# Optimization experiments

Measured on AMD Instinct MI355X. Metric: run time of the kernel, lower is better.

Reference implementation:

```python
import jax, jax.numpy as jnp
import numpy as np

# atom_dict indices
N_IDX, CA_IDX, C_IDX = 0, 1, 2
O4P_IDX, C2P_IDX, C1P_IDX = 11, 14, 15
NA_REF_IDX = 15  # C1'
TOP_K = 30
NUM_RBF = 16
MAX_REL = 32
NUM_POLY = 3
B, L, A = 1, 512, 24


def setup_inputs() -> dict:
    key = jax.random.key(0)
    ks = jax.random.split(key, 8)
    X = 5.0 * jax.random.normal(ks[0], (B, L, A, 3), dtype=jnp.float32)
    mask = jnp.ones((B, L), dtype=jnp.float32)
    R_idx = jnp.broadcast_to(jnp.arange(L, dtype=jnp.int32), (B, L))
    chain_labels = jnp.broadcast_to((jnp.arange(L) // (L // 2)).astype(jnp.int32), (B, L))
    X_m = jnp.ones((B, L, A), dtype=jnp.float32)
    R_polymer_type = jax.random.randint(ks[1], (B, L), 0, NUM_POLY)
    protein_mask = (R_polymer_type == 0).astype(jnp.float32)
    dna_mask = (R_polymer_type == 1).astype(jnp.float32)
    rna_mask = (R_polymer_type == 2).astype(jnp.float32)
    TOTAL_ATOMS = A + 2
    edge_in = 2 * MAX_REL + 2  # placeholder; real edge_in below
    edge_in = NUM_RBF * TOTAL_ATOMS * TOTAL_ATOMS + 16  # 10832
    W_pos = 0.1 * jax.random.normal(ks[2], (16, 2 * MAX_REL + 2), dtype=jnp.float32)
    b_pos = 0.01 * jax.random.normal(ks[3], (16,), dtype=jnp.float32)
    W_edge = 0.02 * jax.random.normal(ks[4], (128, edge_in), dtype=jnp.float32)
    W_node = 0.1 * jax.random.normal(ks[5], (128, NUM_POLY), dtype=jnp.float32)
    gamma_e = jnp.ones((128,), jnp.float32); beta_e = jnp.zeros((128,), jnp.float32)
    gamma_n = jnp.ones((128,), jnp.float32); beta_n = jnp.zeros((128,), jnp.float32)
    return dict(X=X, mask=mask, R_idx=R_idx, chain_labels=chain_labels, X_m=X_m,
                protein_mask=protein_mask, dna_mask=dna_mask, rna_mask=rna_mask,
                R_polymer_type=R_polymer_type, W_pos=W_pos, b_pos=b_pos,
                W_edge=W_edge, W_node=W_node, gamma_e=gamma_e, beta_e=beta_e,
                gamma_n=gamma_n, beta_n=beta_n)


def _get_cb(n, ca, c, wa, wb, wc):
    b = ca - n
    cc = c - ca
    a = jnp.cross(b, cc)
    return wa * a + wb * b + wc * cc + ca


def _layernorm(x, g, b, eps=1e-5):
    m = x.mean(-1, keepdims=True)
    v = ((x - m) ** 2).mean(-1, keepdims=True)
    return (x - m) / jnp.sqrt(v + eps) * g + b


def _dist_topk(Xc, mask):
    # Xc: [B,L,3]
    mask2d = mask[:, None, :] * mask[:, :, None]  # [B,L,L]
    dX = Xc[:, None, :, :] - Xc[:, :, None, :]
    D = mask2d * jnp.sqrt((dX ** 2).sum(-1) + 1e-6)
    D_max = D.max(-1, keepdims=True)
    D_adjust = D + (1.0 - mask2d) * D_max
    negD, E_idx = jax.lax.top_k(-D_adjust, TOP_K)  # smallest distances
    return -negD, E_idx


def reference(X, mask, R_idx, chain_labels, X_m, protein_mask, dna_mask, rna_mask,
              R_polymer_type, W_pos, b_pos, W_edge, W_node, gamma_e, beta_e,
              gamma_n, beta_n):
    Bb, Ll = X.shape[0], X.shape[1]
    Ca = X[:, :, CA_IDX]
    Nb = X[:, :, N_IDX]
    Cc = X[:, :, C_IDX]
    Cb = _get_cb(Nb, Ca, Cc, -0.58273431, 0.56802827, -0.54067466)
    na_ref = X[:, :, NA_REF_IDX]
    N_na = _get_cb(X[:, :, O4P_IDX], X[:, :, C1P_IDX], X[:, :, C2P_IDX],
                   -0.56967352, 0.51055973, -0.53122153)
    aug_X = jnp.concatenate([X, Cb[:, :, None, :], N_na[:, :, None, :]], axis=2)  # [B,L,26,3]
    aug_Xm = jnp.concatenate([X_m, protein_mask[:, :, None],
                              (rna_mask + dna_mask)[:, :, None]], axis=-1)  # [B,L,26]

    _, E_idx = _dist_topk(Ca + na_ref, mask)  # [B,L,K]

    # gather neighbor atoms / masks: [B,L,K,26,3], [B,L,K,26]
    bidx = jnp.arange(Bb)[:, None, None]
    X_g = aug_X[bidx, E_idx]
    Xm_g = aug_Xm[bidx, E_idx]

    # all-atom pairwise distances [B,L,K,26,26]
    Dall = jnp.sqrt(((aug_X[:, :, None, :, None, :] - X_g[:, :, :, None, :, :]) ** 2).sum(-1) + 1e-6)
    D_mu = jnp.linspace(2.0, 22.0, NUM_RBF)
    D_sigma = (22.0 - 2.0) / NUM_RBF
    RBF = jnp.exp(-((Dall[..., None] - D_mu) / D_sigma) ** 2)  # [B,L,K,26,26,16]
    RBF = RBF * aug_Xm[:, :, None, :, None, None] * Xm_g[:, :, :, None, :, None]
    RBF_all = RBF.reshape(Bb, Ll, TOP_K, -1)  # [B,L,K,26*26*16]

    offset = R_idx[:, :, None] - R_idx[:, None, :]  # [B,L,L]
    offset = jnp.take_along_axis(offset, E_idx, axis=2)  # [B,L,K]
    d_chains = (chain_labels[:, :, None] == chain_labels[:, None, :]).astype(jnp.int32)
    E_chains = jnp.take_along_axis(d_chains, E_idx, axis=2)

    d = jnp.clip(offset + MAX_REL, 0, 2 * MAX_REL) * E_chains + (1 - E_chains) * (2 * MAX_REL + 1)
    d_onehot = jax.nn.one_hot(d, 2 * MAX_REL + 2, dtype=jnp.float32)
    E_positional = d_onehot @ W_pos.T + b_pos  # [B,L,K,16]

    E = jnp.concatenate([E_positional, RBF_all], axis=-1)
    E = E @ W_edge.T  # [B,L,K,128]
    E = _layernorm(E, gamma_e, beta_e)

    V = jax.nn.one_hot(R_polymer_type, NUM_POLY, dtype=jnp.float32) @ W_node.T
    V = _layernorm(V, gamma_n, beta_n)
    return V, E, E_idx
```

## Files before the change

### kernel.cpp

```cpp
#include <hip/hip_runtime.h>
#include <stdint.h>


#define NRES   512
#define TOPK   30
#define NATOM  26
#define KTOT   10832
#define NDCP   170
#define MTOT   (NRES*TOPK)
#define NOUT   128
#define KSPLIT 6

#define OFF_AUGX4  0u
#define OFF_EIDX   212992u
#define OFF_WSWZ   274432u
#define OFF_JTAB   1667072u
#define OFF_EPART  4861952u

#define OUT_V     0
#define OUT_E     (NRES*NOUT)
#define OUT_EIDX  (OUT_E + MTOT*NOUT)

typedef __attribute__((ext_vector_type(4))) float f32x4;

#define SA_C   0.96089792702915984f
#define MU0_C  1.9217958540583197f
#define MUS_C  1.2811972360388798f

__device__ __forceinline__ unsigned short f2bf(float f) {
    unsigned u = __builtin_bit_cast(unsigned, f);
    return (unsigned short)((u + 0x7fffu + ((u >> 16) & 1u)) >> 16);
}
__device__ __forceinline__ float bf2f(unsigned short u) {
    return __builtin_bit_cast(float, (unsigned)u << 16);
}
__device__ __forceinline__ float bflo(unsigned u) {
    return __builtin_bit_cast(float, u << 16);
}
__device__ __forceinline__ float bfhi(unsigned u) {
    return __builtin_bit_cast(float, u & 0xffff0000u);
}
__device__ __forceinline__ unsigned long long shfl_xor_u64(unsigned long long v, int m) {
    unsigned lo = (unsigned)v, hi = (unsigned)(v >> 32);
    lo = (unsigned)__shfl_xor((int)lo, m, 64);
    hi = (unsigned)__shfl_xor((int)hi, m, 64);
    return ((unsigned long long)hi << 32) | lo;
}
__device__ __forceinline__ float fexp2(float x) { return __builtin_amdgcn_exp2f(x); }
__device__ __forceinline__ float fsqrtf(float x) { return __builtin_amdgcn_sqrtf(x); }

__device__ __forceinline__ unsigned long long gen8c(float4 xi, float jx, float jy,
                                                    float jz, float mu3, float CC) {
    float dx = xi.x - jx, dy = xi.y - jy, dz = xi.z - jz;
    float d2 = __builtin_fmaf(dx, dx, __builtin_fmaf(dy, dy,
               __builtin_fmaf(dz, dz, 1e-6f)));
    float Ds = fsqrtf(d2) * SA_C;
    Ds = fminf(Ds, 45.0f);
    Ds = (xi.w == 0.0f) ? 45.0f : Ds;
    float u  = Ds - mu3;
    float e3 = fexp2(-(u * u));
    float r  = fexp2(__builtin_fmaf( 2.0f*MUS_C, u, -(MUS_C*MUS_C)));
    float sd = fexp2(__builtin_fmaf(-2.0f*MUS_C, u, -(MUS_C*MUS_C)));
    float e4 = e3*r;  r  *= CC;
    float e5 = e4*r;  r  *= CC;
    float e6 = e5*r;  r  *= CC;
    float e7 = e6*r;
    float e2 = e3*sd; sd *= CC;
    float e1 = e2*sd; sd *= CC;
    float e0 = e1*sd;
    int r0 = __builtin_amdgcn_cvt_pk_fp8_f32(e0, e1, 0, false);
    r0     = __builtin_amdgcn_cvt_pk_fp8_f32(e2, e3, r0, true);
    int r1 = __builtin_amdgcn_cvt_pk_fp8_f32(e4, e5, 0, false);
    r1     = __builtin_amdgcn_cvt_pk_fp8_f32(e6, e7, r1, true);
    return (unsigned long long)(unsigned)r0 | ((unsigned long long)(unsigned)r1 << 32);
}

__global__ __launch_bounds__(256) void kPrep(
    const float* __restrict__ X, const float* __restrict__ Xm,
    const float* __restrict__ prot, const float* __restrict__ dna,
    const float* __restrict__ rna, const int* __restrict__ ptype,
    const float* __restrict__ Wn, const float* __restrict__ gn,
    const float* __restrict__ bn, const float* __restrict__ We,
    char* __restrict__ ws, float* __restrict__ out)
{
    if (blockIdx.x >= NRES) {
        int idx = blockIdx.x - NRES;
        int n = idx / 3;
        int s = (idx - n*3)*256 + threadIdx.x;
        if (s >= 677) return;
        const float* src = We + (size_t)n*KTOT + ((s < 676) ? (16 + s*16) : 0);
        float4 v0 = ((const float4*)src)[0];
        float4 v1 = ((const float4*)src)[1];
        float4 v2 = ((const float4*)src)[2];
        float4 v3 = ((const float4*)src)[3];
        int d = s >> 2, hc = s & 3, h = hc >> 1, cc = hc & 1;
        size_t base = OFF_WSWZ + ((size_t)(d*8 + (n >> 4))*64)*16 + (size_t)cc*8;
        {
            int r0 = __builtin_amdgcn_cvt_pk_fp8_f32(v0.x, v0.y, 0, false);
            r0     = __builtin_amdgcn_cvt_pk_fp8_f32(v0.z, v0.w, r0, true);
            int r1 = __builtin_amdgcn_cvt_pk_fp8_f32(v1.x, v1.y, 0, false);
            r1     = __builtin_amdgcn_cvt_pk_fp8_f32(v1.z, v1.w, r1, true);
            int lane = h*32 + (n & 15);
            *(uint2*)(ws + base + (size_t)lane*16) = make_uint2((unsigned)r0, (unsigned)r1);
        }
        {
            int r0 = __builtin_amdgcn_cvt_pk_fp8_f32(v2.x, v2.y, 0, false);
            r0     = __builtin_amdgcn_cvt_pk_fp8_f32(v2.z, v2.w, r0, true);
            int r1 = __builtin_amdgcn_cvt_pk_fp8_f32(v3.x, v3.y, 0, false);
            r1     = __builtin_amdgcn_cvt_pk_fp8_f32(v3.z, v3.w, r1, true);
            int lane = h*32 + 16 + (n & 15);
            *(uint2*)(ws + base + (size_t)lane*16) = make_uint2((unsigned)r0, (unsigned)r1);
        }
        return;
    }

    const int i = blockIdx.x, t = threadIdx.x;
    if (t >= 128) return;
    float4* augX4 = (float4*)(ws + OFF_AUGX4);
    int*    Eidx  = (int*)(ws + OFF_EIDX);
    const float* Xi = X + i * 72;

    if (t < 26) {
        float x, y, z, mk;
        if (t < 24) {
            x = Xi[t*3]; y = Xi[t*3+1]; z = Xi[t*3+2];
            mk = Xm[i*24 + t];
        } else if (t == 24) {
            float b0 = Xi[3]-Xi[0], b1 = Xi[4]-Xi[1], b2 = Xi[5]-Xi[2];
            float c0 = Xi[6]-Xi[3], c1 = Xi[7]-Xi[4], c2 = Xi[8]-Xi[5];
            float a0 = b1*c2-b2*c1, a1 = b2*c0-b0*c2, a2 = b0*c1-b1*c0;
            x = -0.58273431f*a0 + 0.56802827f*b0 - 0.54067466f*c0 + Xi[3];
            y = -0.58273431f*a1 + 0.56802827f*b1 - 0.54067466f*c1 + Xi[4];
            z = -0.58273431f*a2 + 0.56802827f*b2 - 0.54067466f*c2 + Xi[5];
            mk = prot[i];
        } else {
            const float* O4 = Xi + 33; const float* C1 = Xi + 45; const float* C2 = Xi + 42;
            float b0 = C1[0]-O4[0], b1 = C1[1]-O4[1], b2 = C1[2]-O4[2];
            float c0 = C2[0]-C1[0], c1 = C2[1]-C1[1], c2 = C2[2]-C1[2];
            float a0 = b1*c2-b2*c1, a1 = b2*c0-b0*c2, a2 = b0*c1-b1*c0;
            x = -0.56967352f*a0 + 0.51055973f*b0 - 0.53122153f*c0 + C1[0];
            y = -0.56967352f*a1 + 0.51055973f*b1 - 0.53122153f*c1 + C1[1];
            z = -0.56967352f*a2 + 0.51055973f*b2 - 0.53122153f*c2 + C1[2];
            mk = dna[i] + rna[i];
        }
        augX4[i*26 + t] = make_float4(x, y, z, mk);
    }

    __shared__ float red[4];
    int ty = ptype[i];
    float v = Wn[t*3 + ty];
    float s = v;
    #pragma unroll
    for (int off = 32; off; off >>= 1) s += __shfl_xor(s, off, 64);
    if ((t & 63) == 0) red[t>>6] = s;
    __syncthreads();
    float mean = (red[0] + red[1]) * (1.0f/128.0f);
    float d = v - mean;
    float s2 = d*d;
    #pragma unroll
    for (int off = 32; off; off >>= 1) s2 += __shfl_xor(s2, off, 64);
    if ((t & 63) == 0) red[2 + (t>>6)] = s2;
    __syncthreads();
    float var = (red[2] + red[3]) * (1.0f/128.0f);
    out[OUT_V + i*NOUT + t] = d * rsqrtf(var + 1e-5f) * gn[t] + bn[t];

    if (t >= 64) return;
    const int l = t;
    float xi0 = Xi[3] + Xi[45], xi1 = Xi[4] + Xi[46], xi2 = Xi[5] + Xi[47];
    unsigned long long cand[8];
    #pragma unroll
    for (int sg = 0; sg < 8; sg++) {
        int j = sg*64 + l;
        const float* Xj = X + j*72;
        float c0 = Xj[3] + Xj[45], c1 = Xj[4] + Xj[46], c2 = Xj[5] + Xj[47];
        float dx = xi0 - c0, dy = xi1 - c1, dz = xi2 - c2;
        float dd = __fadd_rn(__fadd_rn(__fadd_rn(__fmul_rn(dx,dx), __fmul_rn(dy,dy)),
                                       __fmul_rn(dz,dz)), 1e-6f);
        float D = sqrtf(dd);
        cand[sg] = ((unsigned long long)__builtin_bit_cast(unsigned, D) << 32) | (unsigned)j;
    }
    for (int m = 0; m < TOPK; m++) {
        unsigned long long k = cand[0];
        #pragma unroll
        for (int sg = 1; sg < 8; sg++) if (cand[sg] < k) k = cand[sg];
        #pragma unroll
        for (int off = 32; off; off >>= 1) {
            unsigned long long o = shfl_xor_u64(k, off);
            if (o < k) k = o;
        }
        if (l == 0) {
            int j = (int)(k & 0xffffffffu);
            Eidx[i*TOPK + m] = j;
            out[OUT_EIDX + i*TOPK + m] = (float)j;
        }
        #pragma unroll
        for (int sg = 0; sg < 8; sg++) if (cand[sg] == k) cand[sg] = ~0ull;
    }
}

__global__ __launch_bounds__(256) void kG(char* __restrict__ ws)
{
    const float4* augX4 = (const float4*)(ws + OFF_AUGX4);
    const int*    Eidx  = (const int*)(ws + OFF_EIDX);
    uint2*        jTab  = (uint2*)(ws + OFF_JTAB);

    const int bx = blockIdx.x, t = threadIdx.x;
    const int rl = t & 127, half = t >> 7;
    const int j = Eidx[bx*128 + rl];
    const float4* Aj = augX4 + j*26;
    #pragma unroll
    for (int aa = 0; aa < 13; aa++) {
        int a = half*13 + aa;
        float4 p = Aj[a];
        float x = p.x, y = p.y, z = p.z;
        if (p.w == 0.0f) { x = -30000.0f; y = -30000.0f; z = -30000.0f; }
        uint2 pk;
        pk.x = (unsigned)f2bf(x) | ((unsigned)f2bf(y) << 16);
        pk.y = (unsigned)f2bf(z);
        jTab[((size_t)bx*26 + a)*128 + rl] = pk;
    }
}

__global__ __launch_bounds__(256, 3) void kC(const int* __restrict__ Ridx,
                                             const int* __restrict__ chain,
                                             const float* __restrict__ Wp,
                                             const float* __restrict__ bp,
                                             char* __restrict__ ws)
{
    const int bx = blockIdx.x, q = blockIdx.y;
    const int t = threadIdx.x, lane = t & 63, w = t >> 6;
    const int mlane = lane & 15, qd = lane >> 4;
    const int h = qd >> 1, fh = qd & 1;

    const float4*     augX4 = (const float4*)(ws + OFF_AUGX4);
    const int*        Eidx  = (const int*)(ws + OFF_EIDX);
    const ulonglong2* gW2   = (const ulonglong2*)(ws + OFF_WSWZ);
    const uint2*      jTab  = (const uint2*)(ws + OFF_JTAB) + (size_t)bx*26*128;
    unsigned short*   Ep    = (unsigned short*)(ws + OFF_EPART)
                            + (size_t)q * MTOT * NOUT;

    const int rl0 = w*32 + mlane, rl1 = rl0 + 16;
    const int r0 = bx*128 + rl0, r1 = r0 + 16;
    const int i0 = r0 / TOPK, i1 = r1 / TOPK;

    const float mu3 = MU0_C + (float)(fh*8 + 3) * MUS_C;
    const float CC  = fexp2(-2.0f * MUS_C * MUS_C);

    const float4* Ai0 = augX4 + i0*26;
    const float4* Ai1 = augX4 + i1*26;

    f32x4 acc0[8], acc1[8];
    #pragma unroll
    for (int nt = 0; nt < 8; nt++) {
        acc0[nt] = (f32x4){0.f,0.f,0.f,0.f};
        acc1[nt] = (f32x4){0.f,0.f,0.f,0.f};
    }

    const int d0 = (q < 2) ? q*29 : (58 + (q-2)*28);
    const int ni = (q < 2) ? 29 : ((q == 5) ? 27 : 28);

    int p0s = 4*d0 + 2*h;
    int a = p0s / 26, rem = p0s - a*26;

    const ulonglong2* Wb = gW2 + (size_t)d0*512 + lane;

    for (int dd = 0; dd < ni; dd++) {
        ulonglong2 b[8];
        #pragma unroll
        for (int nt = 0; nt < 8; nt++) b[nt] = Wb[nt*64];
        Wb += 512;

        uint2 j00 = jTab[(size_t)rem*128 + rl0];
        uint2 j01 = jTab[(size_t)(rem+1)*128 + rl0];
        uint2 j10 = jTab[(size_t)rem*128 + rl1];
        uint2 j11 = jTab[(size_t)(rem+1)*128 + rl1];
        float4 xi0 = Ai0[a], xi1 = Ai1[a];

        unsigned long long a00 = gen8c(xi0, bflo(j00.x), bfhi(j00.x), bflo(j00.y), mu3, CC);
        unsigned long long a01 = gen8c(xi0, bflo(j01.x), bfhi(j01.x), bflo(j01.y), mu3, CC);
        unsigned long long a10 = gen8c(xi1, bflo(j10.x), bfhi(j10.x), bflo(j10.y), mu3, CC);
        unsigned long long a11 = gen8c(xi1, bflo(j11.x), bfhi(j11.x), bflo(j11.y), mu3, CC);

        #pragma unroll
        for (int nt = 0; nt < 8; nt++) {
            acc0[nt] = __builtin_amdgcn_mfma_f32_16x16x32_fp8_fp8((long)a00, (long)b[nt].x, acc0[nt], 0, 0, 0);
            acc0[nt] = __builtin_amdgcn_mfma_f32_16x16x32_fp8_fp8((long)a01, (long)b[nt].y, acc0[nt], 0, 0, 0);
            acc1[nt] = __builtin_amdgcn_mfma_f32_16x16x32_fp8_fp8((long)a10, (long)b[nt].x, acc1[nt], 0, 0, 0);
            acc1[nt] = __builtin_amdgcn_mfma_f32_16x16x32_fp8_fp8((long)a11, (long)b[nt].y, acc1[nt], 0, 0, 0);
        }

        int remn = rem + 4;
        a   += (remn >= 26) ? 1 : 0;
        rem  = (remn >= 26) ? remn - 26 : remn;
    }

    if (q == 5) {
        ulonglong2 b[8];
        #pragma unroll
        for (int nt = 0; nt < 8; nt++) b[nt] = Wb[nt*64];

        int dc0, dc1;
        {
            int j0 = Eidx[r0], j1 = Eidx[r1];
            int off  = Ridx[i0] - Ridx[j0];
            int same = (chain[i0] == chain[j0]);
            int dc = off + 32; dc = dc < 0 ? 0 : (dc > 64 ? 64 : dc);
            dc0 = same ? dc : 65;
            off  = Ridx[i1] - Ridx[j1];
            same = (chain[i1] == chain[j1]);
            dc = off + 32; dc = dc < 0 ? 0 : (dc > 64 ? 64 : dc);
            dc1 = same ? dc : 65;
        }

        unsigned long long a00 = 0, a10 = 0;
        if (h == 0) {
            float e0[8], e1[8];
            #pragma unroll
            for (int ff = 0; ff < 8; ff++) {
                int fc = fh*8 + ff;
                float bv = bp[fc];
                e0[ff] = Wp[fc*66 + dc0] + bv;
                e1[ff] = Wp[fc*66 + dc1] + bv;
            }
            int r0p = __builtin_amdgcn_cvt_pk_fp8_f32(e0[0], e0[1], 0, false);
            r0p     = __builtin_amdgcn_cvt_pk_fp8_f32(e0[2], e0[3], r0p, true);
            int r1p = __builtin_amdgcn_cvt_pk_fp8_f32(e0[4], e0[5], 0, false);
            r1p     = __builtin_amdgcn_cvt_pk_fp8_f32(e0[6], e0[7], r1p, true);
            a00 = (unsigned long long)(unsigned)r0p | ((unsigned long long)(unsigned)r1p << 32);
            r0p = __builtin_amdgcn_cvt_pk_fp8_f32(e1[0], e1[1], 0, false);
            r0p = __builtin_amdgcn_cvt_pk_fp8_f32(e1[2], e1[3], r0p, true);
            r1p = __builtin_amdgcn_cvt_pk_fp8_f32(e1[4], e1[5], 0, false);
            r1p = __builtin_amdgcn_cvt_pk_fp8_f32(e1[6], e1[7], r1p, true);
            a10 = (unsigned long long)(unsigned)r0p | ((unsigned long long)(unsigned)r1p << 32);
        }
        #pragma unroll
        for (int nt = 0; nt < 8; nt++) {
            acc0[nt] = __builtin_amdgcn_mfma_f32_16x16x32_fp8_fp8((long)a00, (long)b[nt].x, acc0[nt], 0, 0, 0);
            acc1[nt] = __builtin_amdgcn_mfma_f32_16x16x32_fp8_fp8((long)a10, (long)b[nt].x, acc1[nt], 0, 0, 0);
        }
    }

    #pragma unroll
    for (int nt = 0; nt < 8; nt++) {
        int col = nt*16 + mlane;
        #pragma unroll
        for (int rr = 0; rr < 4; rr++) {
            int g0 = bx*128 + w*32 + qd*4 + rr;
            Ep[(size_t)g0*NOUT + col]        = f2bf(acc0[nt][rr]);
            Ep[(size_t)(g0+16)*NOUT + col]   = f2bf(acc1[nt][rr]);
        }
    }
}

__global__ __launch_bounds__(256) void kD(const float* __restrict__ ge,
                                          const float* __restrict__ be,
                                          char* __restrict__ ws,
                                          float* __restrict__ out)
{
    const unsigned* Ep = (const unsigned*)(ws + OFF_EPART);
    const int t = threadIdx.x, wv = t >> 6, lane = t & 63;
    const int row = blockIdx.x*4 + wv;
    const size_t qs = (size_t)MTOT * 64;
    size_t b = (size_t)row*64 + lane;

    float v0 = 0.f, v1 = 0.f;
    #pragma unroll
    for (int qq = 0; qq < KSPLIT; qq++) {
        unsigned u = Ep[b + (size_t)qq*qs];
        v0 += bf2f((unsigned short)(u & 0xffffu));
        v1 += bf2f((unsigned short)(u >> 16));
    }

    float S = v0 + v1, Q = v0*v0 + v1*v1;
    #pragma unroll
    for (int off = 32; off; off >>= 1) {
        S += __shfl_xor(S, off, 64);
        Q += __shfl_xor(Q, off, 64);
    }
    float mean = S * (1.0f/128.0f);
    float var  = Q * (1.0f/128.0f) - mean*mean;
    float rstd = rsqrtf(var + 1e-5f);
    float2 o;
    o.x = (v0 - mean) * rstd * ge[2*lane]   + be[2*lane];
    o.y = (v1 - mean) * rstd * ge[2*lane+1] + be[2*lane+1];
    ((float2*)(out + OUT_E))[(size_t)row*64 + lane] = o;
}

extern "C" void kernel_launch(void* const* d_in, const int* in_sizes, int n_in,
                              void* d_out, int out_size, void* d_ws, size_t ws_size,
                              hipStream_t stream)
{
    const float* X     = (const float*)d_in[0];
    const int*   Ridx  = (const int*)d_in[2];
    const int*   chain = (const int*)d_in[3];
    const float* Xm    = (const float*)d_in[4];
    const float* prot  = (const float*)d_in[5];
    const float* dna   = (const float*)d_in[6];
    const float* rna   = (const float*)d_in[7];
    const int*   ptype = (const int*)d_in[8];
    const float* Wp    = (const float*)d_in[9];
    const float* bp    = (const float*)d_in[10];
    const float* We    = (const float*)d_in[11];
    const float* Wn    = (const float*)d_in[12];
    const float* ge    = (const float*)d_in[13];
    const float* be    = (const float*)d_in[14];
    const float* gn    = (const float*)d_in[15];
    const float* bn    = (const float*)d_in[16];
    char* ws = (char*)d_ws;
    float* out = (float*)d_out;

    kPrep<<<dim3(NRES + 384), dim3(256), 0, stream>>>(X, Xm, prot, dna, rna,
            ptype, Wn, gn, bn, We, ws, out);
    kG<<<dim3(MTOT/128), dim3(256), 0, stream>>>(ws);
    kC<<<dim3(MTOT/128, KSPLIT), dim3(256), 0, stream>>>(Ridx, chain, Wp, bp, ws);
    kD<<<dim3(MTOT/4), dim3(256), 0, stream>>>(ge, be, ws, out);
}
```

Baseline: 185.0 us.

## Fuse neighbor-gather kernel into GEMM kernel via LDS tables and prefetch

Drops the separate kG kernel that wrote a bf16-packed neighbor-atom table to global memory. Each kC block now gathers its neighbor and query atom coordinates straight into shared memory, and operands for the next step are prefetched from LDS one iteration ahead. The goal is to remove a kernel launch and a global round-trip for the table. In exchange, the gather is repeated in every one of the KSPLIT blocks sharing a row tile, and the extra LDS use (about 30 KB per block) may limit occupancy against the launch bound of 3.

Result: faster. 174.7 us (-5.5%).

```diff
diff --git a/kernel.cpp b/kernel.cpp
--- a/kernel.cpp
+++ b/kernel.cpp
@@ -14,8 +14,7 @@
 #define OFF_AUGX4  0u
 #define OFF_EIDX   212992u
 #define OFF_WSWZ   274432u
-#define OFF_JTAB   1667072u
-#define OFF_EPART  4861952u
+#define OFF_EPART  1667072u
 
 #define OUT_V     0
 #define OUT_E     (NRES*NOUT)
@@ -198,29 +197,6 @@
     }
 }
 
-__global__ __launch_bounds__(256) void kG(char* __restrict__ ws)
-{
-    const float4* augX4 = (const float4*)(ws + OFF_AUGX4);
-    const int*    Eidx  = (const int*)(ws + OFF_EIDX);
-    uint2*        jTab  = (uint2*)(ws + OFF_JTAB);
-
-    const int bx = blockIdx.x, t = threadIdx.x;
-    const int rl = t & 127, half = t >> 7;
-    const int j = Eidx[bx*128 + rl];
-    const float4* Aj = augX4 + j*26;
-    #pragma unroll
-    for (int aa = 0; aa < 13; aa++) {
-        int a = half*13 + aa;
-        float4 p = Aj[a];
-        float x = p.x, y = p.y, z = p.z;
-        if (p.w == 0.0f) { x = -30000.0f; y = -30000.0f; z = -30000.0f; }
-        uint2 pk;
-        pk.x = (unsigned)f2bf(x) | ((unsigned)f2bf(y) << 16);
-        pk.y = (unsigned)f2bf(z);
-        jTab[((size_t)bx*26 + a)*128 + rl] = pk;
-    }
-}
-
 __global__ __launch_bounds__(256, 3) void kC(const int* __restrict__ Ridx,
                                              const int* __restrict__ chain,
                                              const float* __restrict__ Wp,
@@ -232,22 +208,42 @@
     const int mlane = lane & 15, qd = lane >> 4;
     const int h = qd >> 1, fh = qd & 1;
 
-    const float4*     augX4 = (const float4*)(ws + OFF_AUGX4);
-    const int*        Eidx  = (const int*)(ws + OFF_EIDX);
-    const ulonglong2* gW2   = (const ulonglong2*)(ws + OFF_WSWZ);
-    const uint2*      jTab  = (const uint2*)(ws + OFF_JTAB) + (size_t)bx*26*128;
-    unsigned short*   Ep    = (unsigned short*)(ws + OFF_EPART)
-                            + (size_t)q * MTOT * NOUT;
+    const float4* augX4 = (const float4*)(ws + OFF_AUGX4);
+    const int*    Eidx  = (const int*)(ws + OFF_EIDX);
+    unsigned short* Ep  = (unsigned short*)(ws + OFF_EPART)
+                        + (size_t)q * MTOT * NOUT;
+
+    __shared__ uint2  jT[NATOM * 128];
+    __shared__ float4 iT[160];
+    __shared__ int    JrowS[128];
+
+    if (t < 128) JrowS[t] = Eidx[bx*128 + t];
+    __syncthreads();
+    const int i_base = (bx*128) / TOPK;
+    if (t < 156) {
+        int il = t / 26, a = t - il*26;
+        int gi = i_base + il; gi = gi > 511 ? 511 : gi;
+        iT[t] = augX4[(size_t)gi*26 + a];
+    }
+    for (int wk = t; wk < NATOM*128; wk += 256) {
+        int a = wk >> 7, rl = wk & 127;
+        float4 p = augX4[(size_t)JrowS[rl]*26 + a];
+        float x = p.x, y = p.y, z = p.z;
+        if (p.w == 0.0f) { x = -30000.0f; y = -30000.0f; z = -30000.0f; }
+        uint2 pk;
+        pk.x = (unsigned)f2bf(x) | ((unsigned)f2bf(y) << 16);
+        pk.y = (unsigned)f2bf(z);
+        jT[a*128 + rl] = pk;
+    }
+    __syncthreads();
 
     const int rl0 = w*32 + mlane, rl1 = rl0 + 16;
     const int r0 = bx*128 + rl0, r1 = r0 + 16;
     const int i0 = r0 / TOPK, i1 = r1 / TOPK;
+    const int il0 = (i0 - i_base)*26, il1 = (i1 - i_base)*26;
 
     const float mu3 = MU0_C + (float)(fh*8 + 3) * MUS_C;
     const float CC  = fexp2(-2.0f * MUS_C * MUS_C);
-
-    const float4* Ai0 = augX4 + i0*26;
-    const float4* Ai1 = augX4 + i1*26;
 
     f32x4 acc0[8], acc1[8];
     #pragma unroll
@@ -262,24 +258,38 @@
     int p0s = 4*d0 + 2*h;
     int a = p0s / 26, rem = p0s - a*26;
 
-    const ulonglong2* Wb = gW2 + (size_t)d0*512 + lane;
+    const char* WbA = (const char*)(ws + OFF_WSWZ) + (size_t)d0*8192 + (size_t)lane*16;
+    const char* WbB = WbA + 4096;
+
+    uint2  c00 = jT[rem*128 + rl0], c01 = jT[(rem+1)*128 + rl0];
+    uint2  c10 = jT[rem*128 + rl1], c11 = jT[(rem+1)*128 + rl1];
+    float4 xiA = iT[il0 + a],       xiB = iT[il1 + a];
 
     for (int dd = 0; dd < ni; dd++) {
         ulonglong2 b[8];
         #pragma unroll
-        for (int nt = 0; nt < 8; nt++) b[nt] = Wb[nt*64];
-        Wb += 512;
-
-        uint2 j00 = jTab[(size_t)rem*128 + rl0];
-        uint2 j01 = jTab[(size_t)(rem+1)*128 + rl0];
-        uint2 j10 = jTab[(size_t)rem*128 + rl1];
-        uint2 j11 = jTab[(size_t)(rem+1)*128 + rl1];
-        float4 xi0 = Ai0[a], xi1 = Ai1[a];
-
-        unsigned long long a00 = gen8c(xi0, bflo(j00.x), bfhi(j00.x), bflo(j00.y), mu3, CC);
-        unsigned long long a01 = gen8c(xi0, bflo(j01.x), bfhi(j01.x), bflo(j01.y), mu3, CC);
-        unsigned long long a10 = gen8c(xi1, bflo(j10.x), bfhi(j10.x), bflo(j10.y), mu3, CC);
-        unsigned long long a11 = gen8c(xi1, bflo(j11.x), bfhi(j11.x), bflo(j11.y), mu3, CC);
+        for (int nt = 0; nt < 4; nt++)
+            b[nt] = *(const ulonglong2*)(WbA + nt*1024);
+        #pragma unroll
+        for (int nt = 0; nt < 4; nt++)
+            b[4+nt] = *(const ulonglong2*)(WbB + nt*1024);
+        WbA += 8192; WbB += 8192;
+
+        int remn = rem + 4;
+        int an   = a + (remn >= 26 ? 1 : 0);
+        remn     = (remn >= 26) ? remn - 26 : remn;
+        int ac   = an > 25 ? 25 : an;
+        uint2 n00, n01, n10, n11; float4 nxiA, nxiB;
+        if (dd + 1 < ni) {
+            n00 = jT[remn*128 + rl0]; n01 = jT[(remn+1)*128 + rl0];
+            n10 = jT[remn*128 + rl1]; n11 = jT[(remn+1)*128 + rl1];
+            nxiA = iT[il0 + ac];      nxiB = iT[il1 + ac];
+        }
+
+        unsigned long long a00 = gen8c(xiA, bflo(c00.x), bfhi(c00.x), bflo(c00.y), mu3, CC);
+        unsigned long long a01 = gen8c(xiA, bflo(c01.x), bfhi(c01.x), bflo(c01.y), mu3, CC);
+        unsigned long long a10 = gen8c(xiB, bflo(c10.x), bfhi(c10.x), bflo(c10.y), mu3, CC);
+        unsigned long long a11 = gen8c(xiB, bflo(c11.x), bfhi(c11.x), bflo(c11.y), mu3, CC);
 
         #pragma unroll
         for (int nt = 0; nt < 8; nt++) {
@@ -289,19 +299,25 @@
             acc1[nt] = __builtin_amdgcn_mfma_f32_16x16x32_fp8_fp8((long)a11, (long)b[nt].y, acc1[nt], 0, 0, 0);
         }
 
-        int remn = rem + 4;
-        a   += (remn >= 26) ? 1 : 0;
-        rem  = (remn >= 26) ? remn - 26 : remn;
+        if (dd + 1 < ni) {
+            c00 = n00; c01 = n01; c10 = n10; c11 = n11;
+            xiA = nxiA; xiB = nxiB;
+        }
+        a = an; rem = remn;
     }
 
     if (q == 5) {
         ulonglong2 b[8];
         #pragma unroll
-        for (int nt = 0; nt < 8; nt++) b[nt] = Wb[nt*64];
+        for (int nt = 0; nt < 4; nt++)
+            b[nt] = *(const ulonglong2*)(WbA + nt*1024);
+        #pragma unroll
+        for (int nt = 0; nt < 4; nt++)
+            b[4+nt] = *(const ulonglong2*)(WbB + nt*1024);
 
         int dc0, dc1;
         {
-            int j0 = Eidx[r0], j1 = Eidx[r1];
+            int j0 = JrowS[rl0], j1 = JrowS[rl1];
             int off  = Ridx[i0] - Ridx[j0];
             int same = (chain[i0] == chain[j0]);
             int dc = off + 32; dc = dc < 0 ? 0 : (dc > 64 ? 64 : dc);
@@ -411,7 +427,6 @@
 
     kPrep<<<dim3(NRES + 384), dim3(256), 0, stream>>>(X, Xm, prot, dna, rna,
             ptype, Wn, gn, bn, We, ws, out);
-    kG<<<dim3(MTOT/128), dim3(256), 0, stream>>>(ws);
     kC<<<dim3(MTOT/128, KSPLIT), dim3(256), 0, stream>>>(Ridx, chain, Wp, bp, ws);
     kD<<<dim3(MTOT/4), dim3(256), 0, stream>>>(ge, be, ws, out);
 }
```

## Switch edge GEMM to scaled 16x16x128 FP8 MFMA and fuse neighbor gather into kC

Applied to the files above, without the earlier changes.

Moves the main edge-feature GEMM from 16x16x32 FP8 MFMA to the MI355X scaled 16x16x128 f8f6f4 MFMA. The weight swizzle in kPrep is changed to match, and each lane now generates 16 RBF values per atom pair. The separate kG gather kernel is removed: kC stages neighbor coordinates (bf16-packed) and center-atom coordinates into shared memory per block, with blocks shrunk to 128 threads and 64 rows. This is meant to cut MFMA instruction count, a kernel launch, and a global jTab round-trip. In exchange it adds a shared-memory staging phase per block and a more intricate tail handling for the positional features.

New measurement: 165.9 us. 1.12x faster.

```diff
diff --git a/kernel.cpp b/kernel.cpp
--- a/kernel.cpp
+++ b/kernel.cpp
@@ -6,7 +6,7 @@
 #define TOPK   30
 #define NATOM  26
 #define KTOT   10832
-#define NDCP   170
+#define NBLK128 85
 #define MTOT   (NRES*TOPK)
 #define NOUT   128
 #define KSPLIT 6
@@ -14,18 +14,22 @@
 #define OFF_AUGX4  0u
 #define OFF_EIDX   212992u
 #define OFF_WSWZ   274432u
-#define OFF_JTAB   1667072u
-#define OFF_EPART  4861952u
+#define OFF_EPART  1667072u
 
 #define OUT_V     0
 #define OUT_E     (NRES*NOUT)
 #define OUT_EIDX  (OUT_E + MTOT*NOUT)
 
 typedef __attribute__((ext_vector_type(4))) float f32x4;
-
-#define SA_C   0.96089792702915984f
-#define MU0_C  1.9217958540583197f
-#define MUS_C  1.2811972360388798f
+typedef __attribute__((ext_vector_type(8))) int   i32x8;
+
+#define SA_C    0.96089792702915984f
+#define MU0_C   1.9217958540583197f
+#define MUS_C   1.2811972360388798f
+#define MUS2_C  (MUS_C*MUS_C)
+#define MU3_C   (MU0_C + 3.0f*MUS_C)
+#define MU11_C  (MU0_C + 11.0f*MUS_C)
+#define SCL1    0x7f7f7f7f
 
 __device__ __forceinline__ unsigned short f2bf(float f) {
     unsigned u = __builtin_bit_cast(unsigned, f);
@@ -49,30 +53,42 @@
 __device__ __forceinline__ float fexp2(float x) { return __builtin_amdgcn_exp2f(x); }
 __device__ __forceinline__ float fsqrtf(float x) { return __builtin_amdgcn_sqrtf(x); }
 
-__device__ __forceinline__ unsigned long long gen8c(float4 xi, float jx, float jy,
-                                                    float jz, float mu3, float CC) {
+__device__ __forceinline__ uint4 gen16(float4 xi, float jx, float jy, float jz,
+                                       float CC) {
     float dx = xi.x - jx, dy = xi.y - jy, dz = xi.z - jz;
     float d2 = __builtin_fmaf(dx, dx, __builtin_fmaf(dy, dy,
                __builtin_fmaf(dz, dz, 1e-6f)));
     float Ds = fsqrtf(d2) * SA_C;
     Ds = fminf(Ds, 45.0f);
     Ds = (xi.w == 0.0f) ? 45.0f : Ds;
-    float u  = Ds - mu3;
-    float e3 = fexp2(-(u * u));
-    float r  = fexp2(__builtin_fmaf( 2.0f*MUS_C, u, -(MUS_C*MUS_C)));
-    float sd = fexp2(__builtin_fmaf(-2.0f*MUS_C, u, -(MUS_C*MUS_C)));
-    float e4 = e3*r;  r  *= CC;
-    float e5 = e4*r;  r  *= CC;
-    float e6 = e5*r;  r  *= CC;
-    float e7 = e6*r;
-    float e2 = e3*sd; sd *= CC;
-    float e1 = e2*sd; sd *= CC;
-    float e0 = e1*sd;
-    int r0 = __builtin_amdgcn_cvt_pk_fp8_f32(e0, e1, 0, false);
-    r0     = __builtin_amdgcn_cvt_pk_fp8_f32(e2, e3, r0, true);
-    int r1 = __builtin_amdgcn_cvt_pk_fp8_f32(e4, e5, 0, false);
-    r1     = __builtin_amdgcn_cvt_pk_fp8_f32(e6, e7, r1, true);
-    return (unsigned long long)(unsigned)r0 | ((unsigned long long)(unsigned)r1 << 32);
+    uint4 o;
+    {
+        float u = Ds - MU3_C;
+        float e3 = fexp2(-(u * u));
+        float r  = fexp2(__builtin_fmaf( 2.0f*MUS_C, u, -MUS2_C));
+        float sd = fexp2(__builtin_fmaf(-2.0f*MUS_C, u, -MUS2_C));
+        float e4=e3*r;  r*=CC;  float e5=e4*r;  r*=CC;  float e6=e5*r;  r*=CC;  float e7=e6*r;
+        float e2=e3*sd; sd*=CC; float e1=e2*sd; sd*=CC; float e0=e1*sd;
+        int p = __builtin_amdgcn_cvt_pk_fp8_f32(e0, e1, 0, false);
+        p     = __builtin_amdgcn_cvt_pk_fp8_f32(e2, e3, p, true);
+        int q = __builtin_amdgcn_cvt_pk_fp8_f32(e4, e5, 0, false);
+        q     = __builtin_amdgcn_cvt_pk_fp8_f32(e6, e7, q, true);
+        o.x = (unsigned)p; o.y = (unsigned)q;
+    }
+    {
+        float u = Ds - MU11_C;
+        float e3 = fexp2(-(u * u));
+        float r  = fexp2(__builtin_fmaf( 2.0f*MUS_C, u, -MUS2_C));
+        float sd = fexp2(__builtin_fmaf(-2.0f*MUS_C, u, -MUS2_C));
+        float e4=e3*r;  r*=CC;  float e5=e4*r;  r*=CC;  float e6=e5*r;  r*=CC;  float e7=e6*r;
+        float e2=e3*sd; sd*=CC; float e1=e2*sd; sd*=CC; float e0=e1*sd;
+        int p = __builtin_amdgcn_cvt_pk_fp8_f32(e0, e1, 0, false);
+        p     = __builtin_amdgcn_cvt_pk_fp8_f32(e2, e3, p, true);
+        int q = __builtin_amdgcn_cvt_pk_fp8_f32(e4, e5, 0, false);
+        q     = __builtin_amdgcn_cvt_pk_fp8_f32(e6, e7, q, true);
+        o.z = (unsigned)p; o.w = (unsigned)q;
+    }
+    return o;
 }
 
 __global__ __launch_bounds__(256) void kPrep(
@@ -93,24 +109,20 @@
         float4 v1 = ((const float4*)src)[1];
         float4 v2 = ((const float4*)src)[2];
         float4 v3 = ((const float4*)src)[3];
-        int d = s >> 2, hc = s & 3, h = hc >> 1, cc = hc & 1;
-        size_t base = OFF_WSWZ + ((size_t)(d*8 + (n >> 4))*64)*16 + (size_t)cc*8;
-        {
-            int r0 = __builtin_amdgcn_cvt_pk_fp8_f32(v0.x, v0.y, 0, false);
-            r0     = __builtin_amdgcn_cvt_pk_fp8_f32(v0.z, v0.w, r0, true);
-            int r1 = __builtin_amdgcn_cvt_pk_fp8_f32(v1.x, v1.y, 0, false);
-            r1     = __builtin_amdgcn_cvt_pk_fp8_f32(v1.z, v1.w, r1, true);
-            int lane = h*32 + (n & 15);
-            *(uint2*)(ws + base + (size_t)lane*16) = make_uint2((unsigned)r0, (unsigned)r1);
-        }
-        {
-            int r0 = __builtin_amdgcn_cvt_pk_fp8_f32(v2.x, v2.y, 0, false);
-            r0     = __builtin_amdgcn_cvt_pk_fp8_f32(v2.z, v2.w, r0, true);
-            int r1 = __builtin_amdgcn_cvt_pk_fp8_f32(v3.x, v3.y, 0, false);
-            r1     = __builtin_amdgcn_cvt_pk_fp8_f32(v3.z, v3.w, r1, true);
-            int lane = h*32 + 16 + (n & 15);
-            *(uint2*)(ws + base + (size_t)lane*16) = make_uint2((unsigned)r0, (unsigned)r1);
-        }
+        int d = s >> 3, sl = s & 7, qd2 = sl >> 1, cc = sl & 1;
+        size_t base = OFF_WSWZ
+                    + (((size_t)(d*8 + (n >> 4))*64) + (size_t)(qd2*16 + (n & 15)))*32
+                    + (size_t)cc*16;
+        int r0 = __builtin_amdgcn_cvt_pk_fp8_f32(v0.x, v0.y, 0, false);
+        r0     = __builtin_amdgcn_cvt_pk_fp8_f32(v0.z, v0.w, r0, true);
+        int r1 = __builtin_amdgcn_cvt_pk_fp8_f32(v1.x, v1.y, 0, false);
+        r1     = __builtin_amdgcn_cvt_pk_fp8_f32(v1.z, v1.w, r1, true);
+        int r2 = __builtin_amdgcn_cvt_pk_fp8_f32(v2.x, v2.y, 0, false);
+        r2     = __builtin_amdgcn_cvt_pk_fp8_f32(v2.z, v2.w, r2, true);
+        int r3 = __builtin_amdgcn_cvt_pk_fp8_f32(v3.x, v3.y, 0, false);
+        r3     = __builtin_amdgcn_cvt_pk_fp8_f32(v3.z, v3.w, r3, true);
+        *(uint4*)(ws + base) = make_uint4((unsigned)r0, (unsigned)r1,
+                                          (unsigned)r2, (unsigned)r3);
         return;
     }
 
@@ -198,30 +210,7 @@
     }
 }
 
-__global__ __launch_bounds__(256) void kG(char* __restrict__ ws)
-{
-    const float4* augX4 = (const float4*)(ws + OFF_AUGX4);
-    const int*    Eidx  = (const int*)(ws + OFF_EIDX);
-    uint2*        jTab  = (uint2*)(ws + OFF_JTAB);
-
-    const int bx = blockIdx.x, t = threadIdx.x;
-    const int rl = t & 127, half = t >> 7;
-    const int j = Eidx[bx*128 + rl];
-    const float4* Aj = augX4 + j*26;
-    #pragma unroll
-    for (int aa = 0; aa < 13; aa++) {
-        int a = half*13 + aa;
-        float4 p = Aj[a];
-        float x = p.x, y = p.y, z = p.z;
-        if (p.w == 0.0f) { x = -30000.0f; y = -30000.0f; z = -30000.0f; }
-        uint2 pk;
-        pk.x = (unsigned)f2bf(x) | ((unsigned)f2bf(y) << 16);
-        pk.y = (unsigned)f2bf(z);
-        jTab[((size_t)bx*26 + a)*128 + rl] = pk;
-    }
-}
-
-__global__ __launch_bounds__(256, 3) void kC(const int* __restrict__ Ridx,
+__global__ __launch_bounds__(128, 3) void kC(const int* __restrict__ Ridx,
                                              const int* __restrict__ chain,
                                              const float* __restrict__ Wp,
                                              const float* __restrict__ bp,
@@ -230,24 +219,42 @@
     const int bx = blockIdx.x, q = blockIdx.y;
     const int t = threadIdx.x, lane = t & 63, w = t >> 6;
     const int mlane = lane & 15, qd = lane >> 4;
-    const int h = qd >> 1, fh = qd & 1;
-
-    const float4*     augX4 = (const float4*)(ws + OFF_AUGX4);
-    const int*        Eidx  = (const int*)(ws + OFF_EIDX);
-    const ulonglong2* gW2   = (const ulonglong2*)(ws + OFF_WSWZ);
-    const uint2*      jTab  = (const uint2*)(ws + OFF_JTAB) + (size_t)bx*26*128;
-    unsigned short*   Ep    = (unsigned short*)(ws + OFF_EPART)
-                            + (size_t)q * MTOT * NOUT;
+
+    const float4* augX4 = (const float4*)(ws + OFF_AUGX4);
+    const int*    Eidx  = (const int*)(ws + OFF_EIDX);
+    unsigned short* Ep  = (unsigned short*)(ws + OFF_EPART)
+                        + (size_t)q * MTOT * NOUT;
+
+    __shared__ uint2  jT[NATOM * 65];
+    __shared__ float4 iT[5 * 26];
+    __shared__ int    JrowS[64];
+
+    if (t < 64) JrowS[t] = Eidx[bx*64 + t];
+    __syncthreads();
+    const int i_base = (bx*64) / TOPK;
+    if (t < 5*26) {
+        int il = t / 26, aa = t - il*26;
+        int gi = i_base + il; gi = gi > 511 ? 511 : gi;
+        iT[t] = augX4[(size_t)gi*26 + aa];
+    }
+    for (int wk = t; wk < NATOM*64; wk += 128) {
+        int aa = wk >> 6, rl = wk & 63;
+        float4 p = augX4[(size_t)JrowS[rl]*26 + aa];
+        float x = p.x, y = p.y, z = p.z;
+        if (p.w == 0.0f) { x = -30000.0f; y = -30000.0f; z = -30000.0f; }
+        uint2 pk;
+        pk.x = (unsigned)f2bf(x) | ((unsigned)f2bf(y) << 16);
+        pk.y = (unsigned)f2bf(z);
+        jT[aa*65 + rl] = pk;
+    }
+    __syncthreads();
 
     const int rl0 = w*32 + mlane, rl1 = rl0 + 16;
-    const int r0 = bx*128 + rl0, r1 = r0 + 16;
+    const int r0 = bx*64 + rl0, r1 = r0 + 16;
     const int i0 = r0 / TOPK, i1 = r1 / TOPK;
-
-    const float mu3 = MU0_C + (float)(fh*8 + 3) * MUS_C;
-    const float CC  = fexp2(-2.0f * MUS_C * MUS_C);
-
-    const float4* Ai0 = augX4 + i0*26;
-    const float4* Ai1 = augX4 + i1*26;
+    const int il0 = (i0 - i_base)*26, il1 = (i1 - i_base)*26;
+
+    const float CC = fexp2(-2.0f * MUS2_C);
 
     f32x4 acc0[8], acc1[8];
     #pragma unroll
@@ -256,88 +263,162 @@
         acc1[nt] = (f32x4){0.f,0.f,0.f,0.f};
     }
 
-    const int d0 = (q < 2) ? q*29 : (58 + (q-2)*28);
-    const int ni = (q < 2) ? 29 : ((q == 5) ? 27 : 28);
-
-    int p0s = 4*d0 + 2*h;
-    int a = p0s / 26, rem = p0s - a*26;
-
-    const ulonglong2* Wb = gW2 + (size_t)d0*512 + lane;
-
-    for (int dd = 0; dd < ni; dd++) {
-        ulonglong2 b[8];
-        #pragma unroll
-        for (int nt = 0; nt < 8; nt++) b[nt] = Wb[nt*64];
-        Wb += 512;
-
-        uint2 j00 = jTab[(size_t)rem*128 + rl0];
-        uint2 j01 = jTab[(size_t)(rem+1)*128 + rl0];
-        uint2 j10 = jTab[(size_t)rem*128 + rl1];
-        uint2 j11 = jTab[(size_t)(rem+1)*128 + rl1];
-        float4 xi0 = Ai0[a], xi1 = Ai1[a];
-
-        unsigned long long a00 = gen8c(xi0, bflo(j00.x), bfhi(j00.x), bflo(j00.y), mu3, CC);
-        unsigned long long a01 = gen8c(xi0, bflo(j01.x), bfhi(j01.x), bflo(j01.y), mu3, CC);
-        unsigned long long a10 = gen8c(xi1, bflo(j10.x), bfhi(j10.x), bflo(j10.y), mu3, CC);
-        unsigned long long a11 = gen8c(xi1, bflo(j11.x), bfhi(j11.x), bflo(j11.y), mu3, CC);
-
-        #pragma unroll
-        for (int nt = 0; nt < 8; nt++) {
-            acc0[nt] = __builtin_amdgcn_mfma_f32_16x16x32_fp8_fp8((long)a00, (long)b[nt].x, acc0[nt], 0, 0, 0);
-            acc0[nt] = __builtin_amdgcn_mfma_f32_16x16x32_fp8_fp8((long)a01, (long)b[nt].y, acc0[nt], 0, 0, 0);
-            acc1[nt] = __builtin_amdgcn_mfma_f32_16x16x32_fp8_fp8((long)a10, (long)b[nt].x, acc1[nt], 0, 0, 0);
-            acc1[nt] = __builtin_amdgcn_mfma_f32_16x16x32_fp8_fp8((long)a11, (long)b[nt].y, acc1[nt], 0, 0, 0);
-        }
-
-        int remn = rem + 4;
-        a   += (remn >= 26) ? 1 : 0;
-        rem  = (remn >= 26) ? remn - 26 : remn;
+    const int d0 = (q == 0) ? 0 : (1 + q*14);
+    const int nmain = (q == 0) ? 15 : ((q == 5) ? 13 : 14);
+
+    int s0i = d0*8 + 2*qd;
+    int a = s0i / 26, rem = s0i - a*26;
+
+    const char* Wb = (const char*)(ws + OFF_WSWZ) + (size_t)d0*16384 + (size_t)lane*32;
+
+    for (int dd = 0; dd < nmain; dd++) {
+        i32x8 b0 = *(const i32x8*)(Wb);
+        i32x8 b1 = *(const i32x8*)(Wb + 2048);
+        i32x8 b2 = *(const i32x8*)(Wb + 4096);
+        i32x8 b3 = *(const i32x8*)(Wb + 6144);
+
+        int rem1 = rem + 1, a1 = a;
+        if (rem1 == 26) { rem1 = 0; a1 = a + 1; }
+
+        uint2 jR0a = jT[rem*65  + rl0], jR0b = jT[rem1*65 + rl0];
+        uint2 jR1a = jT[rem*65  + rl1], jR1b = jT[rem1*65 + rl1];
+        float4 xiR0a = iT[il0 + a], xiR0b = iT[il0 + a1];
+        float4 xiR1a = iT[il1 + a], xiR1b = iT[il1 + a1];
+
+        uint4 p0a = gen16(xiR0a, bflo(jR0a.x), bfhi(jR0a.x), bflo(jR0a.y), CC);
+        uint4 p0b = gen16(xiR0b, bflo(jR0b.x), bfhi(jR0b.x), bflo(jR0b.y), CC);
+        uint4 p1a = gen16(xiR1a, bflo(jR1a.x), bfhi(jR1a.x), bflo(jR1a.y), CC);
+        uint4 p1b = gen16(xiR1b, bflo(jR1b.x), bfhi(jR1b.x), bflo(jR1b.y), CC);
+
+        i32x8 A0, A1;
+        A0[0]=p0a.x; A0[1]=p0a.y; A0[2]=p0a.z; A0[3]=p0a.w;
+        A0[4]=p0b.x; A0[5]=p0b.y; A0[6]=p0b.z; A0[7]=p0b.w;
+        A1[0]=p1a.x; A1[1]=p1a.y; A1[2]=p1a.z; A1[3]=p1a.w;
+        A1[4]=p1b.x; A1[5]=p1b.y; A1[6]=p1b.z; A1[7]=p1b.w;
+
+        acc0[0] = __builtin_amdgcn_mfma_scale_f32_16x16x128_f8f6f4(A0, b0, acc0[0], 0, 0, 0, SCL1, 0, SCL1);
+        acc1[0] = __builtin_amdgcn_mfma_scale_f32_16x16x128_f8f6f4(A1, b0, acc1[0], 0, 0, 0, SCL1, 0, SCL1);
+        acc0[1] = __builtin_amdgcn_mfma_scale_f32_16x16x128_f8f6f4(A0, b1, acc0[1], 0, 0, 0, SCL1, 0, SCL1);
+        acc1[1] = __builtin_amdgcn_mfma_scale_f32_16x16x128_f8f6f4(A1, b1, acc1[1], 0, 0, 0, SCL1, 0, SCL1);
+        acc0[2] = __builtin_amdgcn_mfma_scale_f32_16x16x128_f8f6f4(A0, b2, acc0[2], 0, 0, 0, SCL1, 0, SCL1);
+        acc1[2] = __builtin_amdgcn_mfma_scale_f32_16x16x128_f8f6f4(A1, b2, acc1[2], 0, 0, 0, SCL1, 0, SCL1);
+        acc0[3] = __builtin_amdgcn_mfma_scale_f32_16x16x128_f8f6f4(A0, b3, acc0[3], 0, 0, 0, SCL1, 0, SCL1);
+        acc1[3] = __builtin_amdgcn_mfma_scale_f32_16x16x128_f8f6f4(A1, b3, acc1[3], 0, 0, 0, SCL1, 0, SCL1);
+
+        i32x8 b4 = *(const i32x8*)(Wb + 8192);
+        i32x8 b5 = *(const i32x8*)(Wb + 10240);
+        i32x8 b6 = *(const i32x8*)(Wb + 12288);
+        i32x8 b7 = *(const i32x8*)(Wb + 14336);
+
+        acc0[4] = __builtin_amdgcn_mfma_scale_f32_16x16x128_f8f6f4(A0, b4, acc0[4], 0, 0, 0, SCL1, 0, SCL1);
+        acc1[4] = __builtin_amdgcn_mfma_scale_f32_16x16x128_f8f6f4(A1, b4, acc1[4], 0, 0, 0, SCL1, 0, SCL1);
+        acc0[5] = __builtin_amdgcn_mfma_scale_f32_16x16x128_f8f6f4(A0, b5, acc0[5], 0, 0, 0, SCL1, 0, SCL1);
+        acc1[5] = __builtin_amdgcn_mfma_scale_f32_16x16x128_f8f6f4(A1, b5, acc1[5], 0, 0, 0, SCL1, 0, SCL1);
+        acc0[6] = __builtin_amdgcn_mfma_scale_f32_16x16x128_f8f6f4(A0, b6, acc0[6], 0, 0, 0, SCL1, 0, SCL1);
+        acc1[6] = __builtin_amdgcn_mfma_scale_f32_16x16x128_f8f6f4(A1, b6, acc1[6], 0, 0, 0, SCL1, 0, SCL1);
+        acc0[7] = __builtin_amdgcn_mfma_scale_f32_16x16x128_f8f6f4(A0, b7, acc0[7], 0, 0, 0, SCL1, 0, SCL1);
+        acc1[7] = __builtin_amdgcn_mfma_scale_f32_16x16x128_f8f6f4(A1, b7, acc1[7], 0, 0, 0, SCL1, 0, SCL1);
+
+        Wb += 16384;
+        rem += 8;
+        if (rem >= 26) { rem -= 26; a += 1; }
     }
 
     if (q == 5) {
-        ulonglong2 b[8];
-        #pragma unroll
-        for (int nt = 0; nt < 8; nt++) b[nt] = Wb[nt*64];
-
-        int dc0, dc1;
-        {
-            int j0 = Eidx[r0], j1 = Eidx[r1];
-            int off  = Ridx[i0] - Ridx[j0];
-            int same = (chain[i0] == chain[j0]);
-            int dc = off + 32; dc = dc < 0 ? 0 : (dc > 64 ? 64 : dc);
-            dc0 = same ? dc : 65;
-            off  = Ridx[i1] - Ridx[j1];
-            same = (chain[i1] == chain[j1]);
-            dc = off + 32; dc = dc < 0 ? 0 : (dc > 64 ? 64 : dc);
-            dc1 = same ? dc : 65;
-        }
-
-        unsigned long long a00 = 0, a10 = 0;
-        if (h == 0) {
-            float e0[8], e1[8];
+        i32x8 b0 = *(const i32x8*)(Wb);
+        i32x8 b1 = *(const i32x8*)(Wb + 2048);
+        i32x8 b2 = *(const i32x8*)(Wb + 4096);
+        i32x8 b3 = *(const i32x8*)(Wb + 6144);
+
+        int rem1 = rem + 1, a1 = a;
+        if (rem1 == 26) { rem1 = 0; a1 = a + 1; }
+        int ac  = a  > 25 ? 25 : a;
+        int a1c = a1 > 25 ? 25 : a1;
+
+        uint2 jR0a = jT[rem*65  + rl0], jR0b = jT[rem1*65 + rl0];
+        uint2 jR1a = jT[rem*65  + rl1], jR1b = jT[rem1*65 + rl1];
+        float4 xiR0a = iT[il0 + ac], xiR0b = iT[il0 + a1c];
+        float4 xiR1a = iT[il1 + ac], xiR1b = iT[il1 + a1c];
+
+        uint4 p0a = gen16(xiR0a, bflo(jR0a.x), bfhi(jR0a.x), bflo(jR0a.y), CC);
+        uint4 p0b = gen16(xiR0b, bflo(jR0b.x), bfhi(jR0b.x), bflo(jR0b.y), CC);
+        uint4 p1a = gen16(xiR1a, bflo(jR1a.x), bfhi(jR1a.x), bflo(jR1a.y), CC);
+        uint4 p1b = gen16(xiR1b, bflo(jR1b.x), bfhi(jR1b.x), bflo(jR1b.y), CC);
+
+        if (qd == 2) {
+            int dc0, dc1;
+            {
+                int j0 = JrowS[rl0], j1 = JrowS[rl1];
+                int off  = Ridx[i0] - Ridx[j0];
+                int same = (chain[i0] == chain[j0]);
+                int dc = off + 32; dc = dc < 0 ? 0 : (dc > 64 ? 64 : dc);
+                dc0 = same ? dc : 65;
+                off  = Ridx[i1] - Ridx[j1];
+                same = (chain[i1] == chain[j1]);
+                dc = off + 32; dc = dc < 0 ? 0 : (dc > 64 ? 64 : dc);
+                dc1 = same ? dc : 65;
+            }
+            float e0[16], e1[16];
             #pragma unroll
-            for (int ff = 0; ff < 8; ff++) {
-                int fc = fh*8 + ff;
-                float bv = bp[fc];
-                e0[ff] = Wp[fc*66 + dc0] + bv;
-                e1[ff] = Wp[fc*66 + dc1] + bv;
+            for (int f = 0; f < 16; f++) {
+                float bv = bp[f];
+                e0[f] = Wp[f*66 + dc0] + bv;
+                e1[f] = Wp[f*66 + dc1] + bv;
             }
-            int r0p = __builtin_amdgcn_cvt_pk_fp8_f32(e0[0], e0[1], 0, false);
-            r0p     = __builtin_amdgcn_cvt_pk_fp8_f32(e0[2], e0[3], r0p, true);
-            int r1p = __builtin_amdgcn_cvt_pk_fp8_f32(e0[4], e0[5], 0, false);
-            r1p     = __builtin_amdgcn_cvt_pk_fp8_f32(e0[6], e0[7], r1p, true);
-            a00 = (unsigned long long)(unsigned)r0p | ((unsigned long long)(unsigned)r1p << 32);
-            r0p = __builtin_amdgcn_cvt_pk_fp8_f32(e1[0], e1[1], 0, false);
-            r0p = __builtin_amdgcn_cvt_pk_fp8_f32(e1[2], e1[3], r0p, true);
-            r1p = __builtin_amdgcn_cvt_pk_fp8_f32(e1[4], e1[5], 0, false);
-            r1p = __builtin_amdgcn_cvt_pk_fp8_f32(e1[6], e1[7], r1p, true);
-            a10 = (unsigned long long)(unsigned)r0p | ((unsigned long long)(unsigned)r1p << 32);
-        }
-        #pragma unroll
-        for (int nt = 0; nt < 8; nt++) {
-            acc0[nt] = __builtin_amdgcn_mfma_f32_16x16x32_fp8_fp8((long)a00, (long)b[nt].x, acc0[nt], 0, 0, 0);
-            acc1[nt] = __builtin_amdgcn_mfma_f32_16x16x32_fp8_fp8((long)a10, (long)b[nt].x, acc1[nt], 0, 0, 0);
-        }
+            int u0 = __builtin_amdgcn_cvt_pk_fp8_f32(e0[0], e0[1], 0, false);
+            u0     = __builtin_amdgcn_cvt_pk_fp8_f32(e0[2], e0[3], u0, true);
+            int u1 = __builtin_amdgcn_cvt_pk_fp8_f32(e0[4], e0[5], 0, false);
+            u1     = __builtin_amdgcn_cvt_pk_fp8_f32(e0[6], e0[7], u1, true);
+            int u2 = __builtin_amdgcn_cvt_pk_fp8_f32(e0[8], e0[9], 0, false);
+            u2     = __builtin_amdgcn_cvt_pk_fp8_f32(e0[10], e0[11], u2, true);
+            int u3 = __builtin_amdgcn_cvt_pk_fp8_f32(e0[12], e0[13], 0, false);
+            u3     = __builtin_amdgcn_cvt_pk_fp8_f32(e0[14], e0[15], u3, true);
+            p0a = make_uint4((unsigned)u0,(unsigned)u1,(unsigned)u2,(unsigned)u3);
+            u0 = __builtin_amdgcn_cvt_pk_fp8_f32(e1[0], e1[1], 0, false);
+            u0 = __builtin_amdgcn_cvt_pk_fp8_f32(e1[2], e1[3], u0, true);
+            u1 = __builtin_amdgcn_cvt_pk_fp8_f32(e1[4], e1[5], 0, false);
+            u1 = __builtin_amdgcn_cvt_pk_fp8_f32(e1[6], e1[7], u1, true);
+            u2 = __builtin_amdgcn_cvt_pk_fp8_f32(e1[8], e1[9], 0, false);
+            u2 = __builtin_amdgcn_cvt_pk_fp8_f32(e1[10], e1[11], u2, true);
+            u3 = __builtin_amdgcn_cvt_pk_fp8_f32(e1[12], e1[13], 0, false);
+            u3 = __builtin_amdgcn_cvt_pk_fp8_f32(e1[14], e1[15], u3, true);
+            p1a = make_uint4((unsigned)u0,(unsigned)u1,(unsigned)u2,(unsigned)u3);
+            p0b = make_uint4(0,0,0,0);
+            p1b = make_uint4(0,0,0,0);
+        }
+        if (qd == 3) {
+            p0a = make_uint4(0,0,0,0); p0b = make_uint4(0,0,0,0);
+            p1a = make_uint4(0,0,0,0); p1b = make_uint4(0,0,0,0);
+        }
+
+        i32x8 A0, A1;
+        A0[0]=p0a.x; A0[1]=p0a.y; A0[2]=p0a.z; A0[3]=p0a.w;
+        A0[4]=p0b.x; A0[5]=p0b.y; A0[6]=p0b.z; A0[7]=p0b.w;
+        A1[0]=p1a.x; A1[1]=p1a.y; A1[2]=p1a.z; A1[3]=p1a.w;
+        A1[4]=p1b.x; A1[5]=p1b.y; A1[6]=p1b.z; A1[7]=p1b.w;
+
+        acc0[0] = __builtin_amdgcn_mfma_scale_f32_16x16x128_f8f6f4(A0, b0, acc0[0], 0, 0, 0, SCL1, 0, SCL1);
+        acc1[0] = __builtin_amdgcn_mfma_scale_f32_16x16x128_f8f6f4(A1, b0, acc1[0], 0, 0, 0, SCL1, 0, SCL1);
+        acc0[1] = __builtin_amdgcn_mfma_scale_f32_16x16x128_f8f6f4(A0, b1, acc0[1], 0, 0, 0, SCL1, 0, SCL1);
+        acc1[1] = __builtin_amdgcn_mfma_scale_f32_16x16x128_f8f6f4(A1, b1, acc1[1], 0, 0, 0, SCL1, 0, SCL1);
+        acc0[2] = __builtin_amdgcn_mfma_scale_f32_16x16x128_f8f6f4(A0, b2, acc0[2], 0, 0, 0, SCL1, 0, SCL1);
+        acc1[2] = __builtin_amdgcn_mfma_scale_f32_16x16x128_f8f6f4(A1, b2, acc1[2], 0, 0, 0, SCL1, 0, SCL1);
+        acc0[3] = __builtin_amdgcn_mfma_scale_f32_16x16x128_f8f6f4(A0, b3, acc0[3], 0, 0, 0, SCL1, 0, SCL1);
+        acc1[3] = __builtin_amdgcn_mfma_scale_f32_16x16x128_f8f6f4(A1, b3, acc1[3], 0, 0, 0, SCL1, 0, SCL1);
+
+        i32x8 b4 = *(const i32x8*)(Wb + 8192);
+        i32x8 b5 = *(const i32x8*)(Wb + 10240);
+        i32x8 b6 = *(const i32x8*)(Wb + 12288);
+        i32x8 b7 = *(const i32x8*)(Wb + 14336);
+
+        acc0[4] = __builtin_amdgcn_mfma_scale_f32_16x16x128_f8f6f4(A0, b4, acc0[4], 0, 0, 0, SCL1, 0, SCL1);
+        acc1[4] = __builtin_amdgcn_mfma_scale_f32_16x16x128_f8f6f4(A1, b4, acc1[4], 0, 0, 0, SCL1, 0, SCL1);
+        acc0[5] = __builtin_amdgcn_mfma_scale_f32_16x16x128_f8f6f4(A0, b5, acc0[5], 0, 0, 0, SCL1, 0, SCL1);
+        acc1[5] = __builtin_amdgcn_mfma_scale_f32_16x16x128_f8f6f4(A1, b5, acc1[5], 0, 0, 0, SCL1, 0, SCL1);
+        acc0[6] = __builtin_amdgcn_mfma_scale_f32_16x16x128_f8f6f4(A0, b6, acc0[6], 0, 0, 0, SCL1, 0, SCL1);
+        acc1[6] = __builtin_amdgcn_mfma_scale_f32_16x16x128_f8f6f4(A1, b6, acc1[6], 0, 0, 0, SCL1, 0, SCL1);
+        acc0[7] = __builtin_amdgcn_mfma_scale_f32_16x16x128_f8f6f4(A0, b7, acc0[7], 0, 0, 0, SCL1, 0, SCL1);
+        acc1[7] = __builtin_amdgcn_mfma_scale_f32_16x16x128_f8f6f4(A1, b7, acc1[7], 0, 0, 0, SCL1, 0, SCL1);
     }
 
     #pragma unroll
@@ -345,9 +426,9 @@
         int col = nt*16 + mlane;
         #pragma unroll
         for (int rr = 0; rr < 4; rr++) {
-            int g0 = bx*128 + w*32 + qd*4 + rr;
-            Ep[(size_t)g0*NOUT + col]        = f2bf(acc0[nt][rr]);
-            Ep[(size_t)(g0+16)*NOUT + col]   = f2bf(acc1[nt][rr]);
+            int g0 = bx*64 + w*32 + qd*4 + rr;
+            Ep[(size_t)g0*NOUT + col]      = f2bf(acc0[nt][rr]);
+            Ep[(size_t)(g0+16)*NOUT + col] = f2bf(acc1[nt][rr]);
         }
     }
 }
@@ -411,7 +492,6 @@
 
     kPrep<<<dim3(NRES + 384), dim3(256), 0, stream>>>(X, Xm, prot, dna, rna,
             ptype, Wn, gn, bn, We, ws, out);
-    kG<<<dim3(MTOT/128), dim3(256), 0, stream>>>(ws);
-    kC<<<dim3(MTOT/128, KSPLIT), dim3(256), 0, stream>>>(Ridx, chain, Wp, bp, ws);
+    kC<<<dim3(240, KSPLIT), dim3(128), 0, stream>>>(Ridx, chain, Wp, bp, ws);
     kD<<<dim3(MTOT/4), dim3(256), 0, stream>>>(ge, be, ws, out);
 }
```
